# Performance work log

Hardware: AMD Instinct MI355X
Metric: run time of the kernel (lower is better)

## Reference

```python
import jax, jax.numpy as jnp
import numpy as np

B, D, T, H = 2048, 512, 16, 1024   # batch, covariate_dim, treatment_dim, mlp hidden
K, M = 50, 16                       # k_neighbors, manifold_dim


def _mlp(xt, W1, b1, W2, b2):
    # outcome model: [B, D+T] -> [B, 1]
    return jnp.tanh(xt @ W1 + b1) @ W2 + b2


def setup_inputs() -> dict:
    key = jax.random.key(0)
    k0, k1, k2, k3, k4 = jax.random.split(key, 5)
    x = jax.random.normal(k0, (B, D), dtype=jnp.float32)
    t = jax.random.normal(k1, (B, T), dtype=jnp.float32)
    perturbations = jax.random.normal(k2, (B, D), dtype=jnp.float32)
    W1 = jax.random.normal(k3, (D + T, H), dtype=jnp.float32) / np.float32(np.sqrt(D + T))
    b1 = jnp.zeros((H,), dtype=jnp.float32)
    W2 = jax.random.normal(k4, (H, 1), dtype=jnp.float32) / np.float32(np.sqrt(H))
    b2 = jnp.zeros((1,), dtype=jnp.float32)
    return {"x": x, "t": t, "perturbations": perturbations,
            "W1": W1, "b1": b1, "W2": W2, "b2": b2}


def reference(x, t, perturbations, W1, b1, W2, b2):
    # grad of sum(y) w.r.t. x (create_graph analog handled by composing jax.grad)
    def scalar_out(xx):
        return _mlp(jnp.concatenate([xx, t], axis=-1), W1, b1, W2, b2).sum()
    grad_x = jax.grad(scalar_out)(x)                      # [B, D]

    # kNN on perturbations (squared distances preserve topk-smallest ordering)
    sq = jnp.sum(perturbations * perturbations, axis=-1)  # [B]
    d2 = sq[:, None] + sq[None, :] - 2.0 * (perturbations @ perturbations.T)
    _, idx = jax.lax.top_k(-d2, K)                        # [B, K] nearest (incl. self)

    neigh = perturbations[idx]                            # [B, K, D] gather
    centered = neigh - neigh.mean(axis=1, keepdims=True)
    # batched reduced SVD: Vt has shape [B, min(K,D), D]
    _, _, Vt = jnp.linalg.svd(centered, full_matrices=False)
    basis = jnp.swapaxes(Vt[:, :M, :], 1, 2)              # [B, D, M] top-M right sing. vecs

    # projection of grad onto tangent space, summed squared norm
    coef = jnp.einsum('bdm,bd->bm', basis, grad_x)        # [B, M]
    proj = jnp.einsum('bdm,bm->bd', basis, coef)          # [B, D]
    return jnp.sum(proj * proj) / B
```

## Files before the change

kernel.cpp:

```cpp
#include <hip/hip_runtime.h>
#include <math.h>
#include <float.h>

#define B_ 2048
#define D_ 512
#define T_ 16
#define H_ 1024
#define K_ 50
#define M_ 16
#define NSWEEP 1
#define SX_STRIDE 2656
#define SLAB 128
#define SROW 136
#define FS 52

typedef __attribute__((ext_vector_type(8))) short s16x8;
typedef __attribute__((ext_vector_type(4))) float f32x4;

__device__ __forceinline__ float bsum64(float v) {
  #pragma unroll
  for (int o = 1; o < 64; o <<= 1) v += __shfl_xor(v, o);
  return v;
}

__device__ __forceinline__ unsigned bf16_rne(float v) {
  union { float f; unsigned u; } a; a.f = v;
  return (a.u + 0x7FFFu + ((a.u >> 16) & 1u)) >> 16;
}
__device__ __forceinline__ float bf16_val(unsigned h) {
  union { unsigned u; float f; } a; a.u = h << 16;
  return a.f;
}
__device__ __forceinline__ void split_bf16(float v, unsigned short* h, unsigned short* l) {
  unsigned hh = bf16_rne(v);
  *h = (unsigned short)hh;
  *l = (unsigned short)bf16_rne(v - bf16_val(hh));
}

__global__ __launch_bounds__(256)
void conv_xt(const float* __restrict__ x, const float* __restrict__ t,
             unsigned short* __restrict__ xh, unsigned short* __restrict__ xl) {
  const int b = blockIdx.y;
  const int c = blockIdx.x * 256 + threadIdx.x;
  if (c >= 544) return;
  float v = 0.f;
  if (c < 512) v = x[(size_t)b * 512 + c];
  else if (c < 528) v = t[(size_t)b * 16 + (c - 512)];
  unsigned short hh, ll; split_bf16(v, &hh, &ll);
  xh[(size_t)b * 544 + c] = hh;
  xl[(size_t)b * 544 + c] = ll;
}

__global__ __launch_bounds__(256)
void conv_mat(const float* __restrict__ A, unsigned short* __restrict__ h,
              unsigned short* __restrict__ l, int n) {
  int i = blockIdx.x * 256 + threadIdx.x;
  if (i >= n) return;
  unsigned short hh, ll; split_bf16(A[i], &hh, &ll);
  h[i] = hh; l[i] = ll;
}

__global__ __launch_bounds__(256)
void conv_w1t(const float* __restrict__ W1, unsigned short* __restrict__ th,
              unsigned short* __restrict__ tl) {
  __shared__ float tile[32][33];
  const int tx = threadIdx.x & 31, ty = threadIdx.x >> 5;
  const int kb = blockIdx.x * 32, hb = blockIdx.y * 32;
  #pragma unroll
  for (int j = 0; j < 4; j++) {
    int k = kb + ty + j * 8;
    tile[ty + j * 8][tx] = (k < 528) ? W1[(size_t)k * 1024 + hb + tx] : 0.f;
  }
  __syncthreads();
  #pragma unroll
  for (int j = 0; j < 4; j++) {
    int hrow = hb + ty + j * 8;
    float v = tile[tx][ty + j * 8];
    unsigned short hh, ll; split_bf16(v, &hh, &ll);
    th[(size_t)hrow * 544 + kb + tx] = hh;
    tl[(size_t)hrow * 544 + kb + tx] = ll;
  }
}

template <int EPI, int PASSES>
__global__ __launch_bounds__(256)
void mfma_nt(const unsigned short* __restrict__ Ah, const unsigned short* __restrict__ Al, int lda,
             const unsigned short* __restrict__ Bh, const unsigned short* __restrict__ Bl, int ldb,
             int K, float* __restrict__ C, int ldc,
             const float* __restrict__ b1, const float* __restrict__ W2,
             unsigned short* __restrict__ acth, unsigned short* __restrict__ actl) {
  __shared__ unsigned short sAh[64 * 40], sBh[64 * 40];
  __shared__ unsigned short sAl[PASSES == 3 ? 64 * 40 : 16];
  __shared__ unsigned short sBl[PASSES == 3 ? 64 * 40 : 16];
  const int tid = threadIdx.x;
  const int lane = tid & 63, wv = tid >> 6;
  const int wm = wv >> 1, wn = wv & 1;
  const int lr = lane & 15, lq = lane >> 4;
  const int m0 = blockIdx.y * 64, n0 = blockIdx.x * 64;
  const int srow = tid >> 2, sk = (tid & 3) * 8;
  f32x4 acc[2][2];
  #pragma unroll
  for (int mt = 0; mt < 2; mt++)
    #pragma unroll
    for (int nt = 0; nt < 2; nt++)
      #pragma unroll
      for (int i = 0; i < 4; i++) acc[mt][nt][i] = 0.f;

  for (int kb = 0; kb < K; kb += 32) {
    float4 va = *(const float4*)(Ah + (size_t)(m0 + srow) * lda + kb + sk);
    float4 vc = *(const float4*)(Bh + (size_t)(n0 + srow) * ldb + kb + sk);
    float4 vb, vd;
    if (PASSES == 3) {
      vb = *(const float4*)(Al + (size_t)(m0 + srow) * lda + kb + sk);
      vd = *(const float4*)(Bl + (size_t)(n0 + srow) * ldb + kb + sk);
    }
    __syncthreads();
    *(float4*)&sAh[srow * 40 + sk] = va;
    *(float4*)&sBh[srow * 40 + sk] = vc;
    if (PASSES == 3) {
      *(float4*)&sAl[srow * 40 + sk] = vb;
      *(float4*)&sBl[srow * 40 + sk] = vd;
    }
    __syncthreads();
    s16x8 fah[2], fal[2], fbh[2], fbl[2];
    #pragma unroll
    for (int mt = 0; mt < 2; mt++) {
      const int r = wm * 32 + mt * 16 + lr;
      fah[mt] = *(const s16x8*)&sAh[r * 40 + lq * 8];
      if (PASSES == 3) fal[mt] = *(const s16x8*)&sAl[r * 40 + lq * 8];
    }
    #pragma unroll
    for (int nt = 0; nt < 2; nt++) {
      const int r = wn * 32 + nt * 16 + lr;
      fbh[nt] = *(const s16x8*)&sBh[r * 40 + lq * 8];
      if (PASSES == 3) fbl[nt] = *(const s16x8*)&sBl[r * 40 + lq * 8];
    }
    #pragma unroll
    for (int mt = 0; mt < 2; mt++)
      #pragma unroll
      for (int nt = 0; nt < 2; nt++)
        acc[mt][nt] = __builtin_amdgcn_mfma_f32_16x16x32_bf16(fah[mt], fbh[nt], acc[mt][nt], 0, 0, 0);
    if (PASSES == 3) {
      #pragma unroll
      for (int mt = 0; mt < 2; mt++)
        #pragma unroll
        for (int nt = 0; nt < 2; nt++)
          acc[mt][nt] = __builtin_amdgcn_mfma_f32_16x16x32_bf16(fah[mt], fbl[nt], acc[mt][nt], 0, 0, 0);
      #pragma unroll
      for (int mt = 0; mt < 2; mt++)
        #pragma unroll
        for (int nt = 0; nt < 2; nt++)
          acc[mt][nt] = __builtin_amdgcn_mfma_f32_16x16x32_bf16(fal[mt], fbh[nt], acc[mt][nt], 0, 0, 0);
    }
  }

  #pragma unroll
  for (int nt = 0; nt < 2; nt++) {
    const int n = n0 + wn * 32 + nt * 16 + lr;
    float bb = 0.f, ww = 0.f;
    if (EPI == 1) { bb = b1[n]; ww = W2[n]; }
    #pragma unroll
    for (int mt = 0; mt < 2; mt++) {
      #pragma unroll
      for (int r = 0; r < 4; r++) {
        const int m = m0 + wm * 32 + mt * 16 + lq * 4 + r;
        float v = acc[mt][nt][r];
        if (EPI == 0) {
          C[(size_t)m * ldc + n] = v;
        } else if (EPI == 1) {
          float z = v + bb;
          float e = __builtin_amdgcn_exp2f(fabsf(z) * -2.885390082f);
          float rc = __builtin_amdgcn_rcpf(1.f + e);
          float s = 4.f * e * rc * rc * ww;
          unsigned short hh, ll; split_bf16(s, &hh, &ll);
          acth[(size_t)m * ldc + n] = hh;
          actl[(size_t)m * ldc + n] = ll;
        } else {
          unsigned short hh, ll; split_bf16(v, &hh, &ll);
          acth[(size_t)m * ldc + n] = hh;
          actl[(size_t)m * ldc + n] = ll;
        }
      }
    }
  }
}

__global__ __launch_bounds__(256)
void sbuild_kernel(const unsigned short* __restrict__ ph, const unsigned short* __restrict__ pl,
                   const unsigned short* __restrict__ gh, const unsigned short* __restrict__ gl,
                   const int* __restrict__ idx, float* __restrict__ Sx) {
  __shared__ unsigned short sh[64 * SROW];
  __shared__ unsigned short sl[64 * SROW];
  __shared__ int ids[K_];
  const int b = blockIdx.x;
  const int tid = threadIdx.x;
  if (tid < K_) ids[tid] = idx[b * K_ + tid];
  const int lane = tid & 63, wv = tid >> 6;
  const int wm = wv >> 1, wn = wv & 1;
  const int lr = lane & 15, lq = lane >> 4;
  const int strow = tid >> 4, stk = (tid & 15) * 8;
  __syncthreads();

  f32x4 acc[2][2];
  #pragma unroll
  for (int mt = 0; mt < 2; mt++)
    #pragma unroll
    for (int nt = 0; nt < 2; nt++)
      #pragma unroll
      for (int i = 0; i < 4; i++) acc[mt][nt][i] = 0.f;

  for (int kb = 0; kb < 512; kb += SLAB) {
    __syncthreads();
    #pragma unroll
    for (int p = 0; p < 4; p++) {
      const int r = p * 16 + strow;
      if (r < 51) {
        const unsigned short* srch = (r < 50) ? ph + (size_t)ids[r] * 512 : gh + (size_t)b * 512;
        const unsigned short* srcl = (r < 50) ? pl + (size_t)ids[r] * 512 : gl + (size_t)b * 512;
        *(float4*)&sh[r * SROW + stk] = *(const float4*)(srch + kb + stk);
        *(float4*)&sl[r * SROW + stk] = *(const float4*)(srcl + kb + stk);
      }
    }
    __syncthreads();
    #pragma unroll
    for (int kk = 0; kk < SLAB; kk += 32) {
      s16x8 fah[2], fal[2], fbh[2], fbl[2];
      #pragma unroll
      for (int mt = 0; mt < 2; mt++) {
        const int r = wm * 32 + mt * 16 + lr;
        fah[mt] = *(const s16x8*)&sh[r * SROW + kk + lq * 8];
        fal[mt] = *(const s16x8*)&sl[r * SROW + kk + lq * 8];
      }
      #pragma unroll
      for (int nt = 0; nt < 2; nt++) {
        const int r = wn * 32 + nt * 16 + lr;
        fbh[nt] = *(const s16x8*)&sh[r * SROW + kk + lq * 8];
        fbl[nt] = *(const s16x8*)&sl[r * SROW + kk + lq * 8];
      }
      #pragma unroll
      for (int mt = 0; mt < 2; mt++)
        #pragma unroll
        for (int nt = 0; nt < 2; nt++)
          acc[mt][nt] = __builtin_amdgcn_mfma_f32_16x16x32_bf16(fah[mt], fbh[nt], acc[mt][nt], 0, 0, 0);
      #pragma unroll
      for (int mt = 0; mt < 2; mt++)
        #pragma unroll
        for (int nt = 0; nt < 2; nt++)
          acc[mt][nt] = __builtin_amdgcn_mfma_f32_16x16x32_bf16(fah[mt], fbl[nt], acc[mt][nt], 0, 0, 0);
      #pragma unroll
      for (int mt = 0; mt < 2; mt++)
        #pragma unroll
        for (int nt = 0; nt < 2; nt++)
          acc[mt][nt] = __builtin_amdgcn_mfma_f32_16x16x32_bf16(fal[mt], fbh[nt], acc[mt][nt], 0, 0, 0);
    }
  }

  float* Sb = Sx + (size_t)b * SX_STRIDE;
  #pragma unroll
  for (int nt = 0; nt < 2; nt++) {
    const int n = wn * 32 + nt * 16 + lr;
    #pragma unroll
    for (int mt = 0; mt < 2; mt++) {
      #pragma unroll
      for (int r = 0; r < 4; r++) {
        const int m = wm * 32 + mt * 16 + lq * 4 + r;
        if (m < 51 && n < 52) Sb[m * 52 + n] = acc[mt][nt][r];
      }
    }
  }
}

__global__ __launch_bounds__(64)
void sq_kernel(const float* __restrict__ P, float* __restrict__ sq) {
  const int b = blockIdx.x, lane = threadIdx.x;
  const float* pr = P + (size_t)b * 512;
  float s = 0.f;
  #pragma unroll
  for (int i = 0; i < 8; i++) { float v = pr[lane + i * 64]; s += v * v; }
  s = bsum64(s);
  if (lane == 0) sq[b] = s;
}

__device__ __forceinline__ unsigned fkey(float f) {
  unsigned u = __float_as_uint(f);
  return u ^ ((unsigned)((int)u >> 31) | 0x80000000u);
}

__global__ __launch_bounds__(64)
void topk_kernel(const float* __restrict__ G, const float* __restrict__ sq,
                 int* __restrict__ idx) {
  const int b = blockIdx.x, lane = threadIdx.x;
  const float* row = G + (size_t)b * 2048;
  float v[32];
  #pragma unroll
  for (int i = 0; i < 32; i++) {
    const int j = i * 64 + lane;
    v[i] = sq[j] - 2.f * row[j];
  }
  float lmin = v[0]; int lslot = 0;
  #pragma unroll
  for (int i = 1; i < 32; i++) { if (v[i] < lmin) { lmin = v[i]; lslot = i; } }
  unsigned long long lk = ((unsigned long long)fkey(lmin) << 11) | (unsigned)(lslot * 64 + lane);
  for (int it = 0; it < K_; it++) {
    unsigned long long bk = lk;
    #pragma unroll
    for (int o = 1; o < 64; o <<= 1) {
      unsigned long long ok = __shfl_xor(bk, o);
      if (ok < bk) bk = ok;
    }
    const int j = (int)(bk & 0x7FFu);
    if (lane == 0) idx[b * K_ + it] = j;
    if (lane == (j & 63)) {
      v[j >> 6] = FLT_MAX;
      lmin = v[0]; lslot = 0;
      #pragma unroll
      for (int i = 1; i < 32; i++) { if (v[i] < lmin) { lmin = v[i]; lslot = i; } }
      lk = ((unsigned long long)fkey(lmin) << 11) | (unsigned)(lslot * 64 + lane);
    }
  }
}

__global__ __launch_bounds__(64, 2)
void final_kernel(const float* __restrict__ Sx, float* __restrict__ out) {
  __shared__ float cols[64 * FS];
  const int b = blockIdx.x;
  const int lane = threadIdx.x;
  const float* Sb = Sx + (size_t)b * SX_STRIDE;

  float q = (lane < K_) ? Sb[50 * 52 + lane] : 0.f;
  float qm = bsum64(q) * (1.f / K_);
  float w = (lane < K_) ? (q - qm) : 0.f;

  float f[K_];
  #pragma unroll
  for (int r = 0; r < K_; r++)
    f[r] = (lane < K_) ? Sb[r * 52 + lane] : 0.f;

  float cm = 0.f;
  #pragma unroll
  for (int r = 0; r < K_; r++) cm += f[r];
  cm *= (1.f / K_);
  float gs = bsum64(lane < K_ ? cm : 0.f) * (1.f / K_);
  float cs = cm - gs;
  #pragma unroll
  for (int r = 0; r < K_; r++) {
    float rm = __shfl(cm, r);
    if (lane < K_) f[r] -= rm + cs;
  }

  float nrm = 0.f;
  #pragma unroll
  for (int r = 0; r < K_; r++) nrm += f[r] * f[r];

  float* my = &cols[lane * FS];
  #pragma unroll
  for (int k = 0; k < 12; k++) {
    float4 t = {f[4 * k], f[4 * k + 1], f[4 * k + 2], f[4 * k + 3]};
    *(float4*)&my[4 * k] = t;
  }
  {
    float4 t = {f[48], f[49], nrm, w};
    *(float4*)&my[48] = t;
  }

  for (int sweep = 0; sweep < NSWEEP; sweep++) {
    for (int r = 0; r < 49; r++) {
      const int kk = (25 * r) % 49;
      int m;
      if (lane >= K_)      m = lane;
      else if (lane == 49) m = kk;
      else if (lane == kk) m = 49;
      else { m = (r - lane) % 49; if (m < 0) m += 49; }

      const float* pc = &cols[m * FS];
      float y[52];
      #pragma unroll
      for (int k = 0; k < 13; k++) {
        float4 t = *(const float4*)&pc[4 * k];
        y[4 * k] = t.x; y[4 * k + 1] = t.y; y[4 * k + 2] = t.z; y[4 * k + 3] = t.w;
      }
      float onrm = y[50];
      float yw   = y[51];

      float d0 = 0.f, d1 = 0.f, d2 = 0.f, d3 = 0.f;
      #pragma unroll
      for (int r2 = 0; r2 < 48; r2 += 4) {
        d0 += f[r2] * y[r2];
        d1 += f[r2 + 1] * y[r2 + 1];
        d2 += f[r2 + 2] * y[r2 + 2];
        d3 += f[r2 + 3] * y[r2 + 3];
      }
      d0 += f[48] * y[48];
      d1 += f[49] * y[49];
      float dot = (d0 + d1) + (d2 + d3);

      const bool isp = lane < m;
      float alpha = isp ? nrm : onrm;
      float beta  = isp ? onrm : nrm;
      float tau = (beta - alpha) * 0.5f * __builtin_amdgcn_rcpf(dot);
      float sg = (tau >= 0.f) ? 1.f : -1.f;
      float s1 = __builtin_amdgcn_sqrtf(1.f + tau * tau);
      float tt = sg * __builtin_amdgcn_rcpf(fabsf(tau) + s1);
      float cc = __builtin_amdgcn_rsqf(1.f + tt * tt);
      float ssv = tt * cc;
      float sr = isp ? -ssv : ssv;
      if (lane >= K_ || fabsf(dot) < 1e-20f) { cc = 1.f; sr = 0.f; }
      #pragma unroll
      for (int r2 = 0; r2 < K_; r2++) f[r2] = cc * f[r2] + sr * y[r2];
      w = cc * w + sr * yw;
      nrm = cc * cc * nrm + sr * sr * onrm + 2.f * cc * sr * dot;

      #pragma unroll
      for (int k = 0; k < 12; k++) {
        float4 t = {f[4 * k], f[4 * k + 1], f[4 * k + 2], f[4 * k + 3]};
        *(float4*)&my[4 * k] = t;
      }
      float4 t = {f[48], f[49], nrm, w};
      *(float4*)&my[48] = t;
    }
  }

  float n2 = 0.f;
  #pragma unroll
  for (int r2 = 0; r2 < K_; r2++) n2 += f[r2] * f[r2];
  int rank = 0;
  #pragma unroll
  for (int j = 0; j < K_; j++) {
    float vj = __shfl(n2, j);
    rank += (vj > n2 || (vj == n2 && j < lane)) ? 1 : 0;
  }
  float lam = sqrtf(n2);
  float contrib = (lane < K_ && rank < M_) ? (w * w / lam) : 0.f;
  contrib = bsum64(contrib);
  if (lane == 0) atomicAdd(out, contrib * (1.f / B_));
}

extern "C" void kernel_launch(void* const* d_in, const int* in_sizes, int n_in,
                              void* d_out, int out_size, void* d_ws, size_t ws_size,
                              hipStream_t stream) {
  const float* x  = (const float*)d_in[0];
  const float* t  = (const float*)d_in[1];
  const float* P  = (const float*)d_in[2];
  const float* W1 = (const float*)d_in[3];
  const float* b1 = (const float*)d_in[4];
  const float* W2 = (const float*)d_in[5];
  float* out = (float*)d_out;

  float* G    = (float*)d_ws;
  float* Sx   = (float*)d_ws;
  unsigned short* xt_h  = (unsigned short*)(G + (size_t)B_ * B_);
  unsigned short* xt_l  = xt_h  + (size_t)B_ * 544;
  unsigned short* w1t_h = xt_l  + (size_t)B_ * 544;
  unsigned short* w1t_l = w1t_h + (size_t)H_ * 544;
  unsigned short* w1_h  = w1t_l + (size_t)H_ * 544;
  unsigned short* w1_l  = w1_h  + (size_t)528 * H_;
  unsigned short* p_h   = w1_l  + (size_t)528 * H_;
  unsigned short* p_l   = p_h   + (size_t)B_ * D_;
  unsigned short* act_h = p_l   + (size_t)B_ * D_;
  unsigned short* act_l = act_h + (size_t)B_ * H_;
  unsigned short* g_h   = act_l + (size_t)B_ * H_;
  unsigned short* g_l   = g_h   + (size_t)B_ * D_;
  float* sq   = (float*)(g_l + (size_t)B_ * D_);
  int*   idx  = (int*)(sq + B_);

  hipMemsetAsync(d_out, 0, sizeof(float), stream);

  conv_xt<<<dim3(3, B_), 256, 0, stream>>>(x, t, xt_h, xt_l);
  conv_w1t<<<dim3(17, 32), 256, 0, stream>>>(W1, w1t_h, w1t_l);
  conv_mat<<<(528 * H_ + 255) / 256, 256, 0, stream>>>(W1, w1_h, w1_l, 528 * H_);
  conv_mat<<<(B_ * D_ + 255) / 256, 256, 0, stream>>>(P, p_h, p_l, B_ * D_);

  mfma_nt<1, 3><<<dim3(H_ / 64, B_ / 64), 256, 0, stream>>>(
      xt_h, xt_l, 544, w1t_h, w1t_l, 544, 544,
      nullptr, H_, b1, W2, act_h, act_l);
  mfma_nt<2, 3><<<dim3(D_ / 64, B_ / 64), 256, 0, stream>>>(
      act_h, act_l, H_, w1_h, w1_l, H_, H_,
      nullptr, D_, nullptr, nullptr, g_h, g_l);
  mfma_nt<0, 1><<<dim3(B_ / 64, B_ / 64), 256, 0, stream>>>(
      p_h, nullptr, D_, p_h, nullptr, D_, D_,
      G, B_, nullptr, nullptr, nullptr, nullptr);

  sq_kernel<<<B_, 64, 0, stream>>>(P, sq);
  topk_kernel<<<B_, 64, 0, stream>>>(G, sq, idx);
  sbuild_kernel<<<B_, 256, 0, stream>>>(p_h, p_l, g_h, g_l, idx, Sx);
  final_kernel<<<B_, 64, 0, stream>>>(Sx, out);
}
```

Before: 290.4 us.

## Fuse prep conversions with sq norms and use radix-select top-k

Merges the x/t and perturbation bf16 splitting plus the squared-norm computation into one per-row kernel. W1 is now converted in both layouts by a single transpose kernel, and the separate sq_kernel is removed. The top-k kernel replaces 50 iterations of wave-wide argmin with a bitwise radix select on sortable keys followed by ballot-based compaction. The aim is to cut launch count, redundant reads and serial selection latency. The neighbor output order is now by index rather than by distance, which is harmless for the SVD but changes tie-breaking.

```diff
diff --git a/kernel.cpp b/kernel.cpp
--- a/kernel.cpp
+++ b/kernel.cpp
@@ -38,38 +38,52 @@
 }
 
 __global__ __launch_bounds__(256)
-void conv_xt(const float* __restrict__ x, const float* __restrict__ t,
-             unsigned short* __restrict__ xh, unsigned short* __restrict__ xl) {
-  const int b = blockIdx.y;
-  const int c = blockIdx.x * 256 + threadIdx.x;
-  if (c >= 544) return;
-  float v = 0.f;
-  if (c < 512) v = x[(size_t)b * 512 + c];
-  else if (c < 528) v = t[(size_t)b * 16 + (c - 512)];
-  unsigned short hh, ll; split_bf16(v, &hh, &ll);
-  xh[(size_t)b * 544 + c] = hh;
-  xl[(size_t)b * 544 + c] = ll;
+void prep_rows(const float* __restrict__ x, const float* __restrict__ t,
+               const float* __restrict__ P,
+               unsigned short* __restrict__ xh, unsigned short* __restrict__ xl,
+               unsigned short* __restrict__ ph, unsigned short* __restrict__ pl,
+               float* __restrict__ sq) {
+  const int b = blockIdx.x, tid = threadIdx.x;
+  for (int c = tid; c < 544; c += 256) {
+    float v = 0.f;
+    if (c < 512) v = x[(size_t)b * 512 + c];
+    else if (c < 528) v = t[(size_t)b * 16 + (c - 512)];
+    unsigned short hh, ll; split_bf16(v, &hh, &ll);
+    xh[(size_t)b * 544 + c] = hh;
+    xl[(size_t)b * 544 + c] = ll;
+  }
+  float s = 0.f;
+  for (int c = tid; c < 512; c += 256) {
+    float v = P[(size_t)b * 512 + c];
+    s += v * v;
+    unsigned short hh, ll; split_bf16(v, &hh, &ll);
+    ph[(size_t)b * 512 + c] = hh;
+    pl[(size_t)b * 512 + c] = ll;
+  }
+  __shared__ float red[4];
+  s = bsum64(s);
+  if ((tid & 63) == 0) red[tid >> 6] = s;
+  __syncthreads();
+  if (tid == 0) sq[b] = (red[0] + red[1]) + (red[2] + red[3]);
 }
 
 __global__ __launch_bounds__(256)
-void conv_mat(const float* __restrict__ A, unsigned short* __restrict__ h,
-              unsigned short* __restrict__ l, int n) {
-  int i = blockIdx.x * 256 + threadIdx.x;
-  if (i >= n) return;
-  unsigned short hh, ll; split_bf16(A[i], &hh, &ll);
-  h[i] = hh; l[i] = ll;
-}
-
-__global__ __launch_bounds__(256)
-void conv_w1t(const float* __restrict__ W1, unsigned short* __restrict__ th,
-              unsigned short* __restrict__ tl) {
+void conv_w1(const float* __restrict__ W1,
+             unsigned short* __restrict__ th, unsigned short* __restrict__ tl,
+             unsigned short* __restrict__ wh, unsigned short* __restrict__ wl) {
   __shared__ float tile[32][33];
   const int tx = threadIdx.x & 31, ty = threadIdx.x >> 5;
   const int kb = blockIdx.x * 32, hb = blockIdx.y * 32;
   #pragma unroll
   for (int j = 0; j < 4; j++) {
     int k = kb + ty + j * 8;
-    tile[ty + j * 8][tx] = (k < 528) ? W1[(size_t)k * 1024 + hb + tx] : 0.f;
+    float v = (k < 528) ? W1[(size_t)k * 1024 + hb + tx] : 0.f;
+    tile[ty + j * 8][tx] = v;
+    if (k < 528) {
+      unsigned short hh, ll; split_bf16(v, &hh, &ll);
+      wh[(size_t)k * 1024 + hb + tx] = hh;
+      wl[(size_t)k * 1024 + hb + tx] = ll;
+    }
   }
   __syncthreads();
   #pragma unroll
@@ -270,17 +284,6 @@
   }
 }
 
-__global__ __launch_bounds__(64)
-void sq_kernel(const float* __restrict__ P, float* __restrict__ sq) {
-  const int b = blockIdx.x, lane = threadIdx.x;
-  const float* pr = P + (size_t)b * 512;
-  float s = 0.f;
-  #pragma unroll
-  for (int i = 0; i < 8; i++) { float v = pr[lane + i * 64]; s += v * v; }
-  s = bsum64(s);
-  if (lane == 0) sq[b] = s;
-}
-
 __device__ __forceinline__ unsigned fkey(float f) {
   unsigned u = __float_as_uint(f);
   return u ^ ((unsigned)((int)u >> 31) | 0x80000000u);
@@ -291,31 +294,46 @@
                  int* __restrict__ idx) {
   const int b = blockIdx.x, lane = threadIdx.x;
   const float* row = G + (size_t)b * 2048;
-  float v[32];
+  unsigned k[32];
   #pragma unroll
   for (int i = 0; i < 32; i++) {
     const int j = i * 64 + lane;
-    v[i] = sq[j] - 2.f * row[j];
-  }
-  float lmin = v[0]; int lslot = 0;
-  #pragma unroll
-  for (int i = 1; i < 32; i++) { if (v[i] < lmin) { lmin = v[i]; lslot = i; } }
-  unsigned long long lk = ((unsigned long long)fkey(lmin) << 11) | (unsigned)(lslot * 64 + lane);
-  for (int it = 0; it < K_; it++) {
-    unsigned long long bk = lk;
-    #pragma unroll
-    for (int o = 1; o < 64; o <<= 1) {
-      unsigned long long ok = __shfl_xor(bk, o);
-      if (ok < bk) bk = ok;
-    }
-    const int j = (int)(bk & 0x7FFu);
-    if (lane == 0) idx[b * K_ + it] = j;
-    if (lane == (j & 63)) {
-      v[j >> 6] = FLT_MAX;
-      lmin = v[0]; lslot = 0;
-      #pragma unroll
-      for (int i = 1; i < 32; i++) { if (v[i] < lmin) { lmin = v[i]; lslot = i; } }
-      lk = ((unsigned long long)fkey(lmin) << 11) | (unsigned)(lslot * 64 + lane);
+    k[i] = fkey(sq[j] - 2.f * row[j]);
+  }
+  unsigned V = 0;
+  bool exact = false;
+  for (int bit = 31; bit >= 0; bit--) {
+    const unsigned cand = V | (1u << bit);
+    int cnt = 0;
+    #pragma unroll
+    for (int i = 0; i < 32; i++) cnt += (k[i] < cand) ? 1 : 0;
+    #pragma unroll
+    for (int o = 1; o < 64; o <<= 1) cnt += __shfl_xor(cnt, o);
+    if (cnt == K_) { V = cand; exact = true; break; }
+    if (cnt < K_ + 1) V = cand;
+  }
+  int base = 0;
+  #pragma unroll
+  for (int i = 0; i < 32; i++) {
+    const bool p = (k[i] < V);
+    const unsigned long long mask = __ballot(p);
+    if (p) {
+      const int pos = base + __popcll(mask & ((1ull << lane) - 1ull));
+      idx[b * K_ + pos] = i * 64 + lane;
+    }
+    base += __popcll(mask);
+  }
+  if (!exact && base < K_) {
+    #pragma unroll
+    for (int i = 0; i < 32; i++) {
+      if (base >= K_) break;
+      const bool p = (k[i] == V);
+      const unsigned long long mask = __ballot(p);
+      if (p) {
+        const int pos = base + __popcll(mask & ((1ull << lane) - 1ull));
+        if (pos < K_) idx[b * K_ + pos] = i * 64 + lane;
+      }
+      base += __popcll(mask);
     }
   }
 }
@@ -465,10 +483,8 @@
 
   hipMemsetAsync(d_out, 0, sizeof(float), stream);
 
-  conv_xt<<<dim3(3, B_), 256, 0, stream>>>(x, t, xt_h, xt_l);
-  conv_w1t<<<dim3(17, 32), 256, 0, stream>>>(W1, w1t_h, w1t_l);
-  conv_mat<<<(528 * H_ + 255) / 256, 256, 0, stream>>>(W1, w1_h, w1_l, 528 * H_);
-  conv_mat<<<(B_ * D_ + 255) / 256, 256, 0, stream>>>(P, p_h, p_l, B_ * D_);
+  prep_rows<<<B_, 256, 0, stream>>>(x, t, P, xt_h, xt_l, p_h, p_l, sq);
+  conv_w1<<<dim3(17, 32), 256, 0, stream>>>(W1, w1t_h, w1t_l, w1_h, w1_l);
 
   mfma_nt<1, 3><<<dim3(H_ / 64, B_ / 64), 256, 0, stream>>>(
       xt_h, xt_l, 544, w1t_h, w1t_l, 544, 544,
@@ -480,7 +496,6 @@
       p_h, nullptr, D_, p_h, nullptr, D_, D_,
       G, B_, nullptr, nullptr, nullptr, nullptr);
 
-  sq_kernel<<<B_, 64, 0, stream>>>(P, sq);
   topk_kernel<<<B_, 64, 0, stream>>>(G, sq, idx);
   sbuild_kernel<<<B_, 256, 0, stream>>>(p_h, p_l, g_h, g_l, idx, Sx);
   final_kernel<<<B_, 64, 0, stream>>>(Sx, out);
```

Result: faster. 257.9 us (-11.2%).
